# Optimization experiments

Hardware: AMD Instinct MI355X
Metric: run time of the kernel (lower is better)

## Reference

```python
import jax, jax.numpy as jnp
import numpy as np

G, NPG = 100, 500
N = G * NPG            # 50000 nodes, contiguous equal-size graphs
IN, H = 128, 256
L = 3                  # num_layers
K = 3                  # knn k (loop=True -> self included)
E = 16 * N             # 800000 edges

def setup_inputs():
    key = jax.random.key(0)
    k = jax.random.split(key, 8)
    x = jax.random.normal(k[0], (N, IN), jnp.float32)
    batch = jnp.repeat(jnp.arange(G, dtype=jnp.int32), NPG)
    gid = jax.random.randint(k[1], (E,), 0, G)
    src = jax.random.randint(k[2], (E,), 0, NPG) + gid * NPG
    dst = jax.random.randint(k[3], (E,), 0, NPG) + gid * NPG
    edge_index = jnp.stack([src, dst]).astype(jnp.int32)
    def lin(kk, fin, fout):
        return (jax.random.normal(kk, (fin, fout), jnp.float32) / np.sqrt(fin)).astype(jnp.float32)
    inp = dict(x=x, edge_index=edge_index, batch=batch)
    inp["emb_W"] = lin(k[4], IN, H); inp["emb_b"] = jnp.zeros((H,), jnp.float32)
    inp["conv_W"] = jnp.stack([lin(jax.random.fold_in(k[5], i), H, H) for i in range(L)])
    inp["conv_b"] = jnp.zeros((L, H), jnp.float32)
    inp["fconv_W"] = jnp.stack([lin(jax.random.fold_in(k[6], i), H, H) for i in range(L)])
    inp["fconv_b"] = jnp.zeros((L, H), jnp.float32)
    inp["norm_w"] = jnp.ones((L, H), jnp.float32); inp["norm_b"] = jnp.zeros((L, H), jnp.float32); inp["norm_ms"] = jnp.ones((L, H), jnp.float32)
    inp["fnorm_w"] = jnp.ones((L, H), jnp.float32); inp["fnorm_b"] = jnp.zeros((L, H), jnp.float32); inp["fnorm_ms"] = jnp.ones((L, H), jnp.float32)
    inp["gate_W"] = lin(k[7], 2 * H, H); inp["gate_b"] = jnp.zeros((H,), jnp.float32)
    return inp

def _gcn_conv(h, src, dst, W, b):
    # GCNConv: add self loops, symmetric deg^-1/2 normalization
    m = h @ W                                     # [N,H]
    loop = jnp.arange(N, dtype=src.dtype)
    s2 = jnp.concatenate([src, loop]); d2 = jnp.concatenate([dst, loop])
    deg = jax.ops.segment_sum(jnp.ones_like(d2, jnp.float32), d2, num_segments=N)
    dinv = jnp.where(deg > 0, jax.lax.rsqrt(deg), 0.0)
    coef = (dinv[s2] * dinv[d2])[:, None]
    return jax.ops.segment_sum(m[s2] * coef, d2, num_segments=N) + b

def _graph_norm(x, batch, w, b, ms, cnt):
    # PyG GraphNorm: out = w * (x - ms*mean) / sqrt(var + eps) + b, per-graph stats
    mean = jax.ops.segment_sum(x, batch, num_segments=G) / cnt
    out = x - mean[batch] * ms
    var = jax.ops.segment_sum(out * out, batch, num_segments=G) / cnt
    return w * out * jax.lax.rsqrt(var + 1e-5)[batch] + b

def _knn_graph(x):
    # per-graph cosine knn, loop=True (self has sim 1 and is kept)
    xr = x.reshape(G, NPG, -1)
    xn = xr / (jnp.linalg.norm(xr, axis=-1, keepdims=True) + 1e-12)
    sim = jnp.einsum('gnh,gmh->gnm', xn, xn)      # [G,NPG,NPG]
    _, idx = jax.lax.top_k(sim, K)                # [G,NPG,K]
    offs = (jnp.arange(G) * NPG)[:, None, None]
    src = (idx + offs).reshape(-1)
    dst = jnp.broadcast_to(jnp.arange(N).reshape(G, NPG, 1), (G, NPG, K)).reshape(-1)
    return src.astype(jnp.int32), dst.astype(jnp.int32)

def reference(x, edge_index, batch, emb_W, emb_b, conv_W, conv_b, norm_w, norm_b, norm_ms, fconv_W, fconv_b, fnorm_w, fnorm_b, fnorm_ms, gate_W, gate_b):
    cnt = jax.ops.segment_sum(jnp.ones((N,), jnp.float32), batch, num_segments=G)[:, None]
    h = x @ emb_W + emb_b
    fsrc, fdst = _knn_graph(h)
    src, dst = edge_index[0], edge_index[1]
    all_x = []
    for i in range(L - 1):   # eval mode: dropout is identity
        prev = h
        h = _gcn_conv(h, src, dst, conv_W[i], conv_b[i])
        h = jax.nn.leaky_relu(_graph_norm(h, batch, norm_w[i], norm_b[i], norm_ms[i], cnt))
        f = _gcn_conv(h, fsrc, fdst, fconv_W[i], fconv_b[i])
        f = jax.nn.leaky_relu(_graph_norm(f, batch, fnorm_w[i], fnorm_b[i], fnorm_ms[i], cnt))
        gate = jax.nn.sigmoid(jnp.concatenate([h, f], axis=-1) @ gate_W + gate_b)
        h = gate * h + (1.0 - gate) * f + prev
        all_x.append(h)
    # faithful to source: for i in range(L): += pool(all_x[i-1])  (Python negative indexing!)
    gf = jnp.zeros((G, H), jnp.float32)
    for i in range(L):
        gf = gf + jax.ops.segment_sum(all_x[i - 1], batch, num_segments=G) / cnt
    return gf
```

## Files before the change

kernel.cpp:

```cpp
#include <hip/hip_runtime.h>
#include <math.h>

#define NN 50000
#define GG 100
#define NPGc 500
#define HH 256
#define IND 128

typedef __attribute__((ext_vector_type(8))) short short8v;
typedef __attribute__((ext_vector_type(4))) float f32x4;

__device__ __forceinline__ ushort f2bf(float f) {
    union { float f; unsigned u; } v; v.f = f;
    unsigned r = (v.u + 0x7fffu + ((v.u >> 16) & 1u)) >> 16;
    return (ushort)r;
}
__device__ __forceinline__ float bf2f(ushort h) {
    union { unsigned u; float f; } v; v.u = ((unsigned)h) << 16;
    return v.f;
}

__device__ __forceinline__ int swz(int row, int kidx) { return kidx ^ ((row & 7) << 3); }

__global__ void wcvt(const float* __restrict__ src, ushort* __restrict__ dst, int K, int N)
{
    int i = blockIdx.x * 256 + threadIdx.x;
    if (i < K * N) {
        int n = i / K, k = i % K;
        dst[i] = f2bf(src[(size_t)k * N + n]);
    }
}

__global__ __launch_bounds__(256)
void gemm_mfma(const float* __restrict__ A, const float* __restrict__ A2,
               const ushort* __restrict__ Wt, const float* __restrict__ bias,
               float* __restrict__ C, ushort* __restrict__ Cbf,
               int M, int K, int lda, int mode,
               const float* __restrict__ hn, const float* __restrict__ fn,
               const float* __restrict__ prev)
{
    __shared__ ushort As[128][64];
    __shared__ ushort Bs[128][64];
    const int tid = threadIdx.x;
    const int lane = tid & 63;
    const int w = tid >> 6;
    const int wr = (w >> 1) * 64, wc = (w & 1) * 64;
    const int row0 = blockIdx.x * 128, col0 = blockIdx.y * 128;
    const int lr = lane & 15, lk = (lane >> 4) * 8;
    f32x4 acc[4][4] = {};

    for (int k0 = 0; k0 < K; k0 += 64) {
        __syncthreads();
        #pragma unroll
        for (int it = 0; it < 4; ++it) {
            int c = it * 256 + tid;
            int row = c >> 3, col = (c & 7) * 8;
            int gr = row0 + row; if (gr > M - 1) gr = M - 1;
            const float* Ap = A; int kk = k0 + col;
            if (A2 != nullptr && kk >= 256) { Ap = A2; kk -= 256; }
            const float* s = &Ap[(size_t)gr * lda + kk];
            float4 v0 = *(const float4*)s;
            float4 v1 = *(const float4*)(s + 4);
            union { ushort u[8]; int4 q; } pk;
            pk.u[0] = f2bf(v0.x); pk.u[1] = f2bf(v0.y); pk.u[2] = f2bf(v0.z); pk.u[3] = f2bf(v0.w);
            pk.u[4] = f2bf(v1.x); pk.u[5] = f2bf(v1.y); pk.u[6] = f2bf(v1.z); pk.u[7] = f2bf(v1.w);
            *(int4*)&As[row][swz(row, col)] = pk.q;
        }
        #pragma unroll
        for (int it = 0; it < 4; ++it) {
            int c = it * 256 + tid;
            int n = c >> 3, k = (c & 7) * 8;
            *(int4*)&Bs[n][swz(n, k)] = *(const int4*)&Wt[(size_t)(col0 + n) * K + k0 + k];
        }
        __syncthreads();
        #pragma unroll
        for (int ks = 0; ks < 2; ++ks) {
            short8v av[4], bv[4];
            #pragma unroll
            for (int m = 0; m < 4; ++m) {
                int rr = wr + m * 16 + lr;
                av[m] = *(const short8v*)&As[rr][swz(rr, ks * 32 + lk)];
            }
            #pragma unroll
            for (int n = 0; n < 4; ++n) {
                int rr = wc + n * 16 + lr;
                bv[n] = *(const short8v*)&Bs[rr][swz(rr, ks * 32 + lk)];
            }
            #pragma unroll
            for (int m = 0; m < 4; ++m)
                #pragma unroll
                for (int n = 0; n < 4; ++n)
                    acc[m][n] = __builtin_amdgcn_mfma_f32_16x16x32_bf16(av[m], bv[n], acc[m][n], 0, 0, 0);
        }
    }
    const int fr = (lane >> 4) * 4;
    if (mode == 0) {
        #pragma unroll
        for (int n = 0; n < 4; ++n) {
            int col = col0 + wc + n * 16 + lr;
            float bb = bias ? bias[col] : 0.f;
            #pragma unroll
            for (int m = 0; m < 4; ++m) {
                int rbase = row0 + wr + m * 16 + fr;
                #pragma unroll
                for (int r = 0; r < 4; ++r) {
                    int row = rbase + r;
                    if (row < M) C[(size_t)row * HH + col] = acc[m][n][r] + bb;
                }
            }
        }
    } else if (mode == 2) {
        #pragma unroll
        for (int n = 0; n < 4; ++n) {
            int col = col0 + wc + n * 16 + lr;
            float bb = bias ? bias[col] : 0.f;
            #pragma unroll
            for (int m = 0; m < 4; ++m) {
                int rbase = row0 + wr + m * 16 + fr;
                #pragma unroll
                for (int r = 0; r < 4; ++r) {
                    int row = rbase + r;
                    if (row < M) Cbf[(size_t)row * HH + col] = f2bf(acc[m][n][r] + bb);
                }
            }
        }
    } else {
        #pragma unroll
        for (int n = 0; n < 4; ++n) {
            int col = col0 + wc + n * 16 + lr;
            float gb = bias[col];
            #pragma unroll
            for (int m = 0; m < 4; ++m) {
                int rbase = row0 + wr + m * 16 + fr;
                #pragma unroll
                for (int r = 0; r < 4; ++r) {
                    int row = rbase + r;
                    if (row < M) {
                        size_t o = (size_t)row * HH + col;
                        float z = acc[m][n][r] + gb;
                        float s = 1.f / (1.f + expf(-z));
                        C[o] = s * hn[o] + (1.f - s) * fn[o] + prev[o];
                    }
                }
            }
        }
    }
}

__global__ __launch_bounds__(256)
void row_norm_hl(const float* __restrict__ h, ushort* __restrict__ xh, ushort* __restrict__ xl)
{
    int n = blockIdx.x, c = threadIdx.x;
    float v = h[(size_t)n * HH + c];
    __shared__ float red[256];
    red[c] = v * v;
    __syncthreads();
    for (int s = 128; s > 0; s >>= 1) {
        if (c < s) red[c] += red[c + s];
        __syncthreads();
    }
    float norm = sqrtf(red[0]);
    float xn = v / (norm + 1e-12f);
    ushort hi = f2bf(xn);
    xh[(size_t)n * HH + c] = hi;
    xl[(size_t)n * HH + c] = f2bf(xn - bf2f(hi));
}

__device__ __forceinline__ bool tk_better(float va, int ia, float vb, int ib)
{
    return (va > vb) || (va == vb && ia < ib);
}

__device__ __forceinline__ void ins3(float v, int i,
                                     float& a0, int& b0, float& a1, int& b1,
                                     float& a2, int& b2)
{
    if (tk_better(v, i, a0, b0))      { a2 = a1; b2 = b1; a1 = a0; b1 = b0; a0 = v; b0 = i; }
    else if (tk_better(v, i, a1, b1)) { a2 = a1; b2 = b1; a1 = v;  b1 = i; }
    else if (tk_better(v, i, a2, b2)) { a2 = v;  b2 = i; }
}

__device__ __forceinline__ void merge3(float& v0, float& v1, float& v2,
                                       int& i0, int& i1, int& i2, int off)
{
    float w0 = __shfl_xor(v0, off), w1 = __shfl_xor(v1, off), w2 = __shfl_xor(v2, off);
    int   j0 = __shfl_xor(i0, off), j1 = __shfl_xor(i1, off), j2 = __shfl_xor(i2, off);
    float avv[3] = { v0, v1, v2 }, bvv[3] = { w0, w1, w2 };
    int   aii[3] = { i0, i1, i2 }, bii[3] = { j0, j1, j2 };
    float rv[3]; int ri[3];
    int p = 0, q = 0;
    #pragma unroll
    for (int t = 0; t < 3; ++t) {
        bool takeA = tk_better(avv[p], aii[p], bvv[q], bii[q]);
        rv[t] = takeA ? avv[p] : bvv[q];
        ri[t] = takeA ? aii[p] : bii[q];
        if (takeA) ++p; else ++q;
    }
    v0 = rv[0]; v1 = rv[1]; v2 = rv[2];
    i0 = ri[0]; i1 = ri[1]; i2 = ri[2];
}

__global__ __launch_bounds__(256, 1)
void simtopk(const ushort* __restrict__ xnh, const ushort* __restrict__ xnl,
             int* __restrict__ fsrc)
{
    __shared__ ushort Bs[2][2][128][36];
    const int bid = blockIdx.x;
    const int xcd = bid & 7;
    const int rb  = (bid >> 3) & 7;
    const int g   = (bid >> 6) * 8 + xcd;
    if (g >= GG) return;
    const int row0 = rb * 64;
    const int tid  = threadIdx.x;
    const int lane = tid & 63;
    const int w    = tid >> 6;
    const int lr   = lane & 15;
    const int hi4  = lane >> 4;
    const size_t base = (size_t)g * NPGc * HH;

    int arow = row0 + w * 16 + lr; if (arow > NPGc - 1) arow = NPGc - 1;
    const ushort* aph = xnh + base + (size_t)arow * HH + hi4 * 8;
    const ushort* apl = xnl + base + (size_t)arow * HH + hi4 * 8;
    short8v ah[8], al[8];
    #pragma unroll
    for (int kc = 0; kc < 8; ++kc) {
        ah[kc] = *(const short8v*)(aph + kc * 32);
        al[kc] = *(const short8v*)(apl + kc * 32);
    }

    const int scol = tid >> 1;
    const int sq   = (tid & 1) * 2;

    float tv0[4], tv1[4], tv2[4];
    int   ti0[4], ti1[4], ti2[4];
    #pragma unroll
    for (int r = 0; r < 4; ++r) {
        tv0[r] = tv1[r] = tv2[r] = -2.f;
        ti0[r] = ti1[r] = ti2[r] = 0x7fffffff;
    }

    for (int ct = 0; ct < 4; ++ct) {
        const int col0 = ct * 128;
        int gcol = col0 + scol; if (gcol > NPGc - 1) gcol = NPGc - 1;
        const ushort* sph = xnh + base + (size_t)gcol * HH + sq * 8;
        const ushort* spl = xnl + base + (size_t)gcol * HH + sq * 8;

        {
            int4 h0 = *(const int4*)(sph);
            int4 h1 = *(const int4*)(sph + 8);
            int4 l0 = *(const int4*)(spl);
            int4 l1 = *(const int4*)(spl + 8);
            *(int4*)&Bs[0][0][scol][sq * 8]     = h0;
            *(int4*)&Bs[0][0][scol][sq * 8 + 8] = h1;
            *(int4*)&Bs[0][1][scol][sq * 8]     = l0;
            *(int4*)&Bs[0][1][scol][sq * 8 + 8] = l1;
        }
        __syncthreads();

        f32x4 acc[8] = {};
        #pragma unroll
        for (int kc = 0; kc < 8; ++kc) {
            const int cur = kc & 1, nxt = cur ^ 1;
            int4 h0, h1, l0, l1;
            if (kc < 7) {
                const ushort* nh = sph + (kc + 1) * 32;
                const ushort* nl = spl + (kc + 1) * 32;
                h0 = *(const int4*)(nh);
                h1 = *(const int4*)(nh + 8);
                l0 = *(const int4*)(nl);
                l1 = *(const int4*)(nl + 8);
            }
            short8v bh[8], bl[8];
            #pragma unroll
            for (int n = 0; n < 8; ++n) {
                int rr = n * 16 + lr;
                bh[n] = *(const short8v*)&Bs[cur][0][rr][hi4 * 8];
                bl[n] = *(const short8v*)&Bs[cur][1][rr][hi4 * 8];
            }
            #pragma unroll
            for (int n = 0; n < 8; ++n) {
                acc[n] = __builtin_amdgcn_mfma_f32_16x16x32_bf16(ah[kc], bh[n], acc[n], 0, 0, 0);
                acc[n] = __builtin_amdgcn_mfma_f32_16x16x32_bf16(ah[kc], bl[n], acc[n], 0, 0, 0);
                acc[n] = __builtin_amdgcn_mfma_f32_16x16x32_bf16(al[kc], bh[n], acc[n], 0, 0, 0);
            }
            if (kc < 7) {
                *(int4*)&Bs[nxt][0][scol][sq * 8]     = h0;
                *(int4*)&Bs[nxt][0][scol][sq * 8 + 8] = h1;
                *(int4*)&Bs[nxt][1][scol][sq * 8]     = l0;
                *(int4*)&Bs[nxt][1][scol][sq * 8 + 8] = l1;
            }
            __syncthreads();
        }

        #pragma unroll
        for (int n = 0; n < 8; ++n) {
            int col = col0 + n * 16 + lr;
            if (col < NPGc) {
                #pragma unroll
                for (int r = 0; r < 4; ++r)
                    ins3(acc[n][r], col, tv0[r], ti0[r], tv1[r], ti1[r], tv2[r], ti2[r]);
            }
        }
    }

    #pragma unroll
    for (int r = 0; r < 4; ++r) {
        #pragma unroll
        for (int off = 1; off <= 8; off <<= 1)
            merge3(tv0[r], tv1[r], tv2[r], ti0[r], ti1[r], ti2[r], off);
    }

    if (lr == 0) {
        #pragma unroll
        for (int r = 0; r < 4; ++r) {
            int row = row0 + w * 16 + hi4 * 4 + r;
            if (row < NPGc) {
                int rg = g * NPGc + row;
                fsrc[rg * 3 + 0] = g * NPGc + ti0[r];
                fsrc[rg * 3 + 1] = g * NPGc + ti1[r];
                fsrc[rg * 3 + 2] = g * NPGc + ti2[r];
            }
        }
    }
}

__global__ void hist_kernel(const int* __restrict__ dst, int* __restrict__ cnt, int nE)
{
    int e = blockIdx.x * 256 + threadIdx.x;
    if (e < nE) atomicAdd(&cnt[dst[e]], 1);
}

__global__ void scan1_kernel(const int* __restrict__ in, int* __restrict__ out,
                             int* __restrict__ bsum, int n)
{
    __shared__ int sh[256];
    int t = threadIdx.x;
    int i = blockIdx.x * 256 + t;
    int v = (i < n) ? in[i] : 0;
    sh[t] = v;
    __syncthreads();
    for (int s = 1; s < 256; s <<= 1) {
        int tv = (t >= s) ? sh[t - s] : 0;
        __syncthreads();
        sh[t] += tv;
        __syncthreads();
    }
    if (i < n) out[i] = sh[t] - v;
    if (t == 255) bsum[blockIdx.x] = sh[255];
}

__global__ void scan2_kernel(int* __restrict__ bsum, int nb)
{
    __shared__ int sh[256];
    int t = threadIdx.x;
    int v = (t < nb) ? bsum[t] : 0;
    sh[t] = v;
    __syncthreads();
    for (int s = 1; s < 256; s <<= 1) {
        int tv = (t >= s) ? sh[t - s] : 0;
        __syncthreads();
        sh[t] += tv;
        __syncthreads();
    }
    if (t < nb) bsum[t] = sh[t] - v;
}

__global__ void scan3_kernel(int* __restrict__ out, const int* __restrict__ bsum, int n)
{
    int i = blockIdx.x * 256 + threadIdx.x;
    if (i < n) out[i] += bsum[blockIdx.x];
}

__global__ void fill_kernel(const int* __restrict__ src, const int* __restrict__ dst,
                            const int* __restrict__ row_ptr, int* __restrict__ cursor,
                            int* __restrict__ sorted_src, int nE)
{
    int e = blockIdx.x * 256 + threadIdx.x;
    if (e < nE) {
        int d = dst[e];
        int pos = row_ptr[d] + atomicAdd(&cursor[d], 1);
        sorted_src[pos] = src[e];
    }
}

__global__ void dinv_kernel(const int* __restrict__ cnt, float* __restrict__ dinv, int n)
{
    int i = blockIdx.x * 256 + threadIdx.x;
    if (i < n) dinv[i] = rsqrtf((float)cnt[i] + 1.0f);
}

__global__ __launch_bounds__(256)
void gcn_gather(const ushort* __restrict__ m, const int* __restrict__ row_ptr,
                const int* __restrict__ cnt, const int* __restrict__ srcs,
                const float* __restrict__ dinv, const float* __restrict__ bias,
                float* __restrict__ out)
{
    int bid = blockIdx.x;
    int xcd = bid & 7, idx = bid >> 3;
    int g = xcd + 8 * (idx / NPGc);
    if (g >= GG) return;
    int n = g * NPGc + (idx % NPGc);
    int c = threadIdx.x;
    float dn = dinv[n];
    float acc = bf2f(m[(size_t)n * HH + c]) * dn;
    int s0 = row_ptr[n], e0 = s0 + cnt[n];
    for (int e = s0; e < e0; ++e) {
        int s = srcs[e];
        acc += bf2f(m[(size_t)s * HH + c]) * dinv[s];
    }
    out[(size_t)n * HH + c] = acc * dn + bias[c];
}

__global__ __launch_bounds__(256)
void fgcn_gather(const ushort* __restrict__ m, const int* __restrict__ fsrc,
                 const float* __restrict__ bias, float* __restrict__ out)
{
    int bid = blockIdx.x;
    int xcd = bid & 7, idx = bid >> 3;
    int g = xcd + 8 * (idx / NPGc);
    if (g >= GG) return;
    int n = g * NPGc + (idx % NPGc);
    int c = threadIdx.x;
    int s0 = fsrc[n * 3], s1 = fsrc[n * 3 + 1], s2 = fsrc[n * 3 + 2];
    float acc = bf2f(m[(size_t)n * HH + c]) + bf2f(m[(size_t)s0 * HH + c])
              + bf2f(m[(size_t)s1 * HH + c]) + bf2f(m[(size_t)s2 * HH + c]);
    out[(size_t)n * HH + c] = 0.25f * acc + bias[c];
}

__global__ __launch_bounds__(256)
void norm_stats(const float* __restrict__ x, float* __restrict__ S1, float* __restrict__ S2)
{
    int g = blockIdx.x, chunk = blockIdx.y, c = threadIdx.x;
    int r0 = chunk * 63, r1 = min(r0 + 63, NPGc);
    float s1 = 0.f, s2 = 0.f;
    for (int r = r0; r < r1; ++r) {
        float v = x[((size_t)(g * NPGc + r)) * HH + c];
        s1 += v; s2 += v * v;
    }
    atomicAdd(&S1[g * HH + c], s1);
    atomicAdd(&S2[g * HH + c], s2);
}

__global__ __launch_bounds__(256)
void norm_apply(float* __restrict__ x, const float* __restrict__ S1, const float* __restrict__ S2,
                const float* __restrict__ w, const float* __restrict__ b,
                const float* __restrict__ ms)
{
    int n = blockIdx.x, c = threadIdx.x;
    int g = n / NPGc;
    size_t o = (size_t)n * HH + c;
    float v = x[o];
    float mean = S1[g * HH + c] / (float)NPGc;
    float mm = mean * ms[c];
    float var = S2[g * HH + c] / (float)NPGc - 2.f * mm * mean + mm * mm;
    float outv = w[c] * (v - mm) * rsqrtf(var + 1e-5f) + b[c];
    x[o] = outv > 0.f ? outv : 0.01f * outv;
}

__global__ __launch_bounds__(256)
void pool_kernel(const float* __restrict__ X0, const float* __restrict__ X1,
                 float* __restrict__ out)
{
    int g = blockIdx.x, c = threadIdx.x;
    float s0 = 0.f, s1 = 0.f;
    for (int r = 0; r < NPGc; ++r) {
        size_t o = ((size_t)(g * NPGc + r)) * HH + c;
        s0 += X0[o];
        s1 += X1[o];
    }
    out[g * HH + c] = (s0 + 2.f * s1) / (float)NPGc;
}

__global__ void sentinel_kernel(float* out, int n)
{
    int i = blockIdx.x * 256 + threadIdx.x;
    if (i < n) out[i] = 12345.0f;
}

extern "C" void kernel_launch(void* const* d_in, const int* in_sizes, int n_in,
                              void* d_out, int out_size, void* d_ws, size_t ws_size,
                              hipStream_t stream)
{
    const float* x       = (const float*)d_in[0];
    const int* edge_idx  = (const int*)d_in[1];
    const float* emb_W   = (const float*)d_in[3];
    const float* emb_b   = (const float*)d_in[4];
    const float* conv_W  = (const float*)d_in[5];
    const float* conv_b  = (const float*)d_in[6];
    const float* fconv_W = (const float*)d_in[7];
    const float* fconv_b = (const float*)d_in[8];
    const float* norm_w  = (const float*)d_in[9];
    const float* norm_b  = (const float*)d_in[10];
    const float* norm_ms = (const float*)d_in[11];
    const float* fnorm_w = (const float*)d_in[12];
    const float* fnorm_b = (const float*)d_in[13];
    const float* fnorm_ms= (const float*)d_in[14];
    const float* gate_W  = (const float*)d_in[15];
    const float* gate_b  = (const float*)d_in[16];

    const int E = in_sizes[1] / 2;
    const int* esrc = edge_idx;
    const int* edst = edge_idx + E;

    const size_t NHf = (size_t)NN * HH;
    char* p = (char*)d_ws;
    auto alloc = [&](size_t bytes) { char* r = p; p += (bytes + 255) & ~(size_t)255; return r; };
    float* B0 = (float*)alloc(NHf * 4);
    float* B1 = (float*)alloc(NHf * 4);
    float* B2 = (float*)alloc(NHf * 4);
    float* B3 = (float*)alloc(NHf * 4);
    ushort* xnh = (ushort*)B2;
    ushort* xnl = xnh + NHf;
    ushort* msgbf = (ushort*)alloc(NHf * 2);
    int* sorted_src = (int*)alloc((size_t)E * 4);
    int* row_ptr    = (int*)alloc((size_t)NN * 4);
    int* deg_cnt    = (int*)alloc((size_t)NN * 4);
    int* cursor     = (int*)alloc((size_t)NN * 4);
    float* dinv     = (float*)alloc((size_t)NN * 4);
    int* fsrc       = (int*)alloc((size_t)NN * 3 * 4);
    float* S1       = (float*)alloc((size_t)GG * HH * 4);
    float* S2       = (float*)alloc((size_t)GG * HH * 4);
    int* bsum       = (int*)alloc(1024);
    ushort* wts     = (ushort*)alloc((size_t)425984 * 2);
    size_t needed = (size_t)(p - (char*)d_ws);
    if (ws_size < needed) {
        sentinel_kernel<<<(out_size + 255) / 256, 256, 0, stream>>>((float*)d_out, out_size);
        return;
    }
    ushort* embWt   = wts;
    ushort* convWt0 = wts + 32768;
    ushort* convWt1 = wts + 32768 + 65536;
    ushort* fconvWt0 = wts + 163840;
    ushort* fconvWt1 = wts + 163840 + 65536;
    ushort* gateWt  = wts + 294912;

    const int nScanB = (NN + 255) / 256;
    const int gatherGrid = 8 * 13 * NPGc;

    hipMemsetAsync(deg_cnt, 0, (size_t)NN * 4, stream);
    hipMemsetAsync(cursor, 0, (size_t)NN * 4, stream);

    wcvt<<<(32768 + 255) / 256, 256, 0, stream>>>(emb_W, embWt, IND, HH);
    wcvt<<<(65536 + 255) / 256, 256, 0, stream>>>(conv_W, convWt0, HH, HH);
    wcvt<<<(65536 + 255) / 256, 256, 0, stream>>>(conv_W + 65536, convWt1, HH, HH);
    wcvt<<<(65536 + 255) / 256, 256, 0, stream>>>(fconv_W, fconvWt0, HH, HH);
    wcvt<<<(65536 + 255) / 256, 256, 0, stream>>>(fconv_W + 65536, fconvWt1, HH, HH);
    wcvt<<<(131072 + 255) / 256, 256, 0, stream>>>(gate_W, gateWt, 2 * HH, HH);

    dim3 ggrid((NN + 127) / 128, 2);
    gemm_mfma<<<ggrid, 256, 0, stream>>>(x, nullptr, embWt, emb_b, B0, nullptr,
                                         NN, IND, IND, 0, nullptr, nullptr, nullptr);

    hist_kernel<<<(E + 255) / 256, 256, 0, stream>>>(edst, deg_cnt, E);
    scan1_kernel<<<nScanB, 256, 0, stream>>>(deg_cnt, row_ptr, bsum, NN);
    scan2_kernel<<<1, 256, 0, stream>>>(bsum, nScanB);
    scan3_kernel<<<nScanB, 256, 0, stream>>>(row_ptr, bsum, NN);
    fill_kernel<<<(E + 255) / 256, 256, 0, stream>>>(esrc, edst, row_ptr, cursor, sorted_src, E);
    dinv_kernel<<<(NN + 255) / 256, 256, 0, stream>>>(deg_cnt, dinv, NN);

    row_norm_hl<<<NN, 256, 0, stream>>>(B0, xnh, xnl);
    simtopk<<<832, 256, 0, stream>>>(xnh, xnl, fsrc);

    float* h  = B0;
    float* mb = B1;
    dim3 ngrid(GG, 8);
    for (int i = 0; i < 2; ++i) {
        const ushort* Wc = (i == 0) ? convWt0 : convWt1;
        const ushort* Wf = (i == 0) ? fconvWt0 : fconvWt1;
        const float* bc  = conv_b  + (size_t)i * HH;
        const float* bf  = fconv_b + (size_t)i * HH;
        gemm_mfma<<<ggrid, 256, 0, stream>>>(h, nullptr, Wc, nullptr, nullptr, msgbf,
                                             NN, HH, HH, 2, nullptr, nullptr, nullptr);
        gcn_gather<<<gatherGrid, 256, 0, stream>>>(msgbf, row_ptr, deg_cnt, sorted_src,
                                                   dinv, bc, B2);
        hipMemsetAsync(S1, 0, (size_t)2 * GG * HH * 4, stream);
        norm_stats<<<ngrid, 256, 0, stream>>>(B2, S1, S2);
        norm_apply<<<NN, 256, 0, stream>>>(B2, S1, S2, norm_w + i * HH, norm_b + i * HH,
                                           norm_ms + i * HH);
        gemm_mfma<<<ggrid, 256, 0, stream>>>(B2, nullptr, Wf, nullptr, nullptr, msgbf,
                                             NN, HH, HH, 2, nullptr, nullptr, nullptr);
        fgcn_gather<<<gatherGrid, 256, 0, stream>>>(msgbf, fsrc, bf, B3);
        hipMemsetAsync(S1, 0, (size_t)2 * GG * HH * 4, stream);
        norm_stats<<<ngrid, 256, 0, stream>>>(B3, S1, S2);
        norm_apply<<<NN, 256, 0, stream>>>(B3, S1, S2, fnorm_w + i * HH, fnorm_b + i * HH,
                                           fnorm_ms + i * HH);
        gemm_mfma<<<ggrid, 256, 0, stream>>>(B2, B3, gateWt, gate_b, mb, nullptr,
                                             NN, 2 * HH, HH, 1, B2, B3, h);
        float* t = h; h = mb; mb = t;
    }
    pool_kernel<<<GG, 256, 0, stream>>>(mb, h, (float*)d_out);
}
```

Measured before the change: 1.296 ms.

## Restructure kNN similarity GEMM into LDS-staged swizzled K-tiles with two blocks per CU

The simtopk kernel no longer keeps the whole A row fragment (hi and lo bf16 splits over K=256) in registers with a double-buffered B ring. Both A and B tiles are now staged through XOR-swizzled shared memory in K chunks of 64, and launch bounds allow two blocks per CU. This is meant to cut register pressure and LDS bank conflicts so occupancy can rise. In exchange the A tile is reloaded from global memory once per column tile, and prefetch overlap is lost because each K chunk is loaded and then consumed between two barriers.

```diff
diff --git a/kernel.cpp b/kernel.cpp
--- a/kernel.cpp
+++ b/kernel.cpp
@@ -200,11 +200,12 @@
     i0 = ri[0]; i1 = ri[1]; i2 = ri[2];
 }
 
-__global__ __launch_bounds__(256, 1)
+__global__ __launch_bounds__(256, 2)
 void simtopk(const ushort* __restrict__ xnh, const ushort* __restrict__ xnl,
              int* __restrict__ fsrc)
 {
-    __shared__ ushort Bs[2][2][128][36];
+    __shared__ ushort Ash[64][64], Asl[64][64];
+    __shared__ ushort Bsh[128][64], Bsl[128][64];
     const int bid = blockIdx.x;
     const int xcd = bid & 7;
     const int rb  = (bid >> 3) & 7;
@@ -216,20 +217,8 @@
     const int w    = tid >> 6;
     const int lr   = lane & 15;
     const int hi4  = lane >> 4;
+    const int lk   = hi4 * 8;
     const size_t base = (size_t)g * NPGc * HH;
-
-    int arow = row0 + w * 16 + lr; if (arow > NPGc - 1) arow = NPGc - 1;
-    const ushort* aph = xnh + base + (size_t)arow * HH + hi4 * 8;
-    const ushort* apl = xnl + base + (size_t)arow * HH + hi4 * 8;
-    short8v ah[8], al[8];
-    #pragma unroll
-    for (int kc = 0; kc < 8; ++kc) {
-        ah[kc] = *(const short8v*)(aph + kc * 32);
-        al[kc] = *(const short8v*)(apl + kc * 32);
-    }
-
-    const int scol = tid >> 1;
-    const int sq   = (tid & 1) * 2;
 
     float tv0[4], tv1[4], tv2[4];
     int   ti0[4], ti1[4], ti2[4];
@@ -241,84 +230,73 @@
 
     for (int ct = 0; ct < 4; ++ct) {
         const int col0 = ct * 128;
-        int gcol = col0 + scol; if (gcol > NPGc - 1) gcol = NPGc - 1;
-        const ushort* sph = xnh + base + (size_t)gcol * HH + sq * 8;
-        const ushort* spl = xnl + base + (size_t)gcol * HH + sq * 8;
-
-        {
-            int4 h0 = *(const int4*)(sph);
-            int4 h1 = *(const int4*)(sph + 8);
-            int4 l0 = *(const int4*)(spl);
-            int4 l1 = *(const int4*)(spl + 8);
-            *(int4*)&Bs[0][0][scol][sq * 8]     = h0;
-            *(int4*)&Bs[0][0][scol][sq * 8 + 8] = h1;
-            *(int4*)&Bs[0][1][scol][sq * 8]     = l0;
-            *(int4*)&Bs[0][1][scol][sq * 8 + 8] = l1;
-        }
-        __syncthreads();
-
         f32x4 acc[8] = {};
-        #pragma unroll
-        for (int kc = 0; kc < 8; ++kc) {
-            const int cur = kc & 1, nxt = cur ^ 1;
-            int4 h0, h1, l0, l1;
-            if (kc < 7) {
-                const ushort* nh = sph + (kc + 1) * 32;
-                const ushort* nl = spl + (kc + 1) * 32;
-                h0 = *(const int4*)(nh);
-                h1 = *(const int4*)(nh + 8);
-                l0 = *(const int4*)(nl);
-                l1 = *(const int4*)(nl + 8);
-            }
-            short8v bh[8], bl[8];
+        for (int k0 = 0; k0 < HH; k0 += 64) {
+            __syncthreads();
+            #pragma unroll
+            for (int it = 0; it < 2; ++it) {
+                int flat = it * 256 + tid;
+                int row = flat >> 3, col = (flat & 7) * 8;
+                int grow = row0 + row; if (grow > NPGc - 1) grow = NPGc - 1;
+                size_t o = base + (size_t)grow * HH + k0 + col;
+                *(int4*)&Ash[row][swz(row, col)] = *(const int4*)(xnh + o);
+                *(int4*)&Asl[row][swz(row, col)] = *(const int4*)(xnl + o);
+            }
+            #pragma unroll
+            for (int it = 0; it < 4; ++it) {
+                int flat = it * 256 + tid;
+                int row = flat >> 3, col = (flat & 7) * 8;
+                int gcol = col0 + row; if (gcol > NPGc - 1) gcol = NPGc - 1;
+                size_t o = base + (size_t)gcol * HH + k0 + col;
+                *(int4*)&Bsh[row][swz(row, col)] = *(const int4*)(xnh + o);
+                *(int4*)&Bsl[row][swz(row, col)] = *(const int4*)(xnl + o);
+            }
+            __syncthreads();
+            #pragma unroll
+            for (int ks = 0; ks < 2; ++ks) {
+                const int ra = w * 16 + lr;
+                short8v ah = *(const short8v*)&Ash[ra][swz(ra, ks * 32 + lk)];
+                short8v al = *(const short8v*)&Asl[ra][swz(ra, ks * 32 + lk)];
+                #pragma unroll
+                for (int n = 0; n < 8; ++n) {
+                    const int rbn = n * 16 + lr;
+                    short8v bh = *(const short8v*)&Bsh[rbn][swz(rbn, ks * 32 + lk)];
+                    short8v bl = *(const short8v*)&Bsl[rbn][swz(rbn, ks * 32 + lk)];
+                    acc[n] = __builtin_amdgcn_mfma_f32_16x16x32_bf16(ah, bh, acc[n], 0, 0, 0);
+                    acc[n] = __builtin_amdgcn_mfma_f32_16x16x32_bf16(ah, bl, acc[n], 0, 0, 0);
+                    acc[n] = __builtin_amdgcn_mfma_f32_16x16x32_bf16(al, bh, acc[n], 0, 0, 0);
+                }
+            }
+        }
+        #pragma unroll
+        for (int r = 0; r < 4; ++r) {
+            float a0 = tv0[r], a1 = tv1[r], a2 = tv2[r];
+            int   b0 = ti0[r], b1 = ti1[r], b2 = ti2[r];
             #pragma unroll
             for (int n = 0; n < 8; ++n) {
-                int rr = n * 16 + lr;
-                bh[n] = *(const short8v*)&Bs[cur][0][rr][hi4 * 8];
-                bl[n] = *(const short8v*)&Bs[cur][1][rr][hi4 * 8];
-            }
-            #pragma unroll
-            for (int n = 0; n < 8; ++n) {
-                acc[n] = __builtin_amdgcn_mfma_f32_16x16x32_bf16(ah[kc], bh[n], acc[n], 0, 0, 0);
-                acc[n] = __builtin_amdgcn_mfma_f32_16x16x32_bf16(ah[kc], bl[n], acc[n], 0, 0, 0);
-                acc[n] = __builtin_amdgcn_mfma_f32_16x16x32_bf16(al[kc], bh[n], acc[n], 0, 0, 0);
-            }
-            if (kc < 7) {
-                *(int4*)&Bs[nxt][0][scol][sq * 8]     = h0;
-                *(int4*)&Bs[nxt][0][scol][sq * 8 + 8] = h1;
-                *(int4*)&Bs[nxt][1][scol][sq * 8]     = l0;
-                *(int4*)&Bs[nxt][1][scol][sq * 8 + 8] = l1;
-            }
-            __syncthreads();
-        }
-
-        #pragma unroll
-        for (int n = 0; n < 8; ++n) {
-            int col = col0 + n * 16 + lr;
-            if (col < NPGc) {
-                #pragma unroll
-                for (int r = 0; r < 4; ++r)
-                    ins3(acc[n][r], col, tv0[r], ti0[r], tv1[r], ti1[r], tv2[r], ti2[r]);
-            }
+                int col = col0 + n * 16 + lr;
+                if (col < NPGc)
+                    ins3(acc[n][r], col, a0, b0, a1, b1, a2, b2);
+            }
+            tv0[r] = a0; tv1[r] = a1; tv2[r] = a2;
+            ti0[r] = b0; ti1[r] = b1; ti2[r] = b2;
         }
     }
 
     #pragma unroll
     for (int r = 0; r < 4; ++r) {
+        float a0 = tv0[r], a1 = tv1[r], a2 = tv2[r];
+        int   b0 = ti0[r], b1 = ti1[r], b2 = ti2[r];
         #pragma unroll
         for (int off = 1; off <= 8; off <<= 1)
-            merge3(tv0[r], tv1[r], tv2[r], ti0[r], ti1[r], ti2[r], off);
-    }
-
-    if (lr == 0) {
-        #pragma unroll
-        for (int r = 0; r < 4; ++r) {
+            merge3(a0, a1, a2, b0, b1, b2, off);
+        if (lr == 0) {
             int row = row0 + w * 16 + hi4 * 4 + r;
             if (row < NPGc) {
                 int rg = g * NPGc + row;
-                fsrc[rg * 3 + 0] = g * NPGc + ti0[r];
-                fsrc[rg * 3 + 1] = g * NPGc + ti1[r];
-                fsrc[rg * 3 + 2] = g * NPGc + ti2[r];
+                fsrc[rg * 3 + 0] = g * NPGc + b0;
+                fsrc[rg * 3 + 1] = g * NPGc + b1;
+                fsrc[rg * 3 + 2] = g * NPGc + b2;
             }
         }
     }
```

Result: slower. 1.322 ms (+2.0%).

## Store intermediate activations in bf16 and replace norm atomics with partial sums

Applied to the files above, without the earlier changes.

Intermediate activations (GCN gather outputs, normalized features, gated layer outputs) are now stored as bf16 instead of fp32. The GEMM reads bf16 inputs directly with no conversion, which roughly halves memory traffic across the gather, norm, gate and pool kernels. GraphNorm statistics are written as per-chunk partial sums that norm_apply reduces, removing the atomics and memsets. The topk insertion loop is also reordered per row. The cost is extra rounding to bf16 on stored activations, including the residual path.

```diff
diff --git a/kernel.cpp b/kernel.cpp
--- a/kernel.cpp
+++ b/kernel.cpp
@@ -32,12 +32,12 @@
 }
 
 __global__ __launch_bounds__(256)
-void gemm_mfma(const float* __restrict__ A, const float* __restrict__ A2,
+void gemm_mfma(const void* __restrict__ Av, const void* __restrict__ A2v, int abf,
                const ushort* __restrict__ Wt, const float* __restrict__ bias,
                float* __restrict__ C, ushort* __restrict__ Cbf,
                int M, int K, int lda, int mode,
-               const float* __restrict__ hn, const float* __restrict__ fn,
-               const float* __restrict__ prev)
+               const ushort* __restrict__ hn, const ushort* __restrict__ fn,
+               const void* __restrict__ prevv, int prevbf)
 {
     __shared__ ushort As[128][64];
     __shared__ ushort Bs[128][64];
@@ -56,15 +56,23 @@
             int c = it * 256 + tid;
             int row = c >> 3, col = (c & 7) * 8;
             int gr = row0 + row; if (gr > M - 1) gr = M - 1;
-            const float* Ap = A; int kk = k0 + col;
-            if (A2 != nullptr && kk >= 256) { Ap = A2; kk -= 256; }
-            const float* s = &Ap[(size_t)gr * lda + kk];
-            float4 v0 = *(const float4*)s;
-            float4 v1 = *(const float4*)(s + 4);
-            union { ushort u[8]; int4 q; } pk;
-            pk.u[0] = f2bf(v0.x); pk.u[1] = f2bf(v0.y); pk.u[2] = f2bf(v0.z); pk.u[3] = f2bf(v0.w);
-            pk.u[4] = f2bf(v1.x); pk.u[5] = f2bf(v1.y); pk.u[6] = f2bf(v1.z); pk.u[7] = f2bf(v1.w);
-            *(int4*)&As[row][swz(row, col)] = pk.q;
+            int kk = k0 + col;
+            if (abf) {
+                const ushort* Ap = (const ushort*)Av;
+                if (A2v != nullptr && kk >= 256) { Ap = (const ushort*)A2v; kk -= 256; }
+                *(int4*)&As[row][swz(row, col)] =
+                    *(const int4*)&Ap[(size_t)gr * lda + kk];
+            } else {
+                const float* Ap = (const float*)Av;
+                if (A2v != nullptr && kk >= 256) { Ap = (const float*)A2v; kk -= 256; }
+                const float* s = &Ap[(size_t)gr * lda + kk];
+                float4 v0 = *(const float4*)s;
+                float4 v1 = *(const float4*)(s + 4);
+                union { ushort u[8]; int4 q; } pk;
+                pk.u[0] = f2bf(v0.x); pk.u[1] = f2bf(v0.y); pk.u[2] = f2bf(v0.z); pk.u[3] = f2bf(v0.w);
+                pk.u[4] = f2bf(v1.x); pk.u[5] = f2bf(v1.y); pk.u[6] = f2bf(v1.z); pk.u[7] = f2bf(v1.w);
+                *(int4*)&As[row][swz(row, col)] = pk.q;
+            }
         }
         #pragma unroll
         for (int it = 0; it < 4; ++it) {
@@ -139,7 +147,11 @@
                         size_t o = (size_t)row * HH + col;
                         float z = acc[m][n][r] + gb;
                         float s = 1.f / (1.f + expf(-z));
-                        C[o] = s * hn[o] + (1.f - s) * fn[o] + prev[o];
+                        float hv = bf2f(hn[o]);
+                        float fv = bf2f(fn[o]);
+                        float pv = prevbf ? bf2f(((const ushort*)prevv)[o])
+                                          : ((const float*)prevv)[o];
+                        Cbf[o] = f2bf(s * hv + (1.f - s) * fv + pv);
                     }
                 }
             }
@@ -293,32 +305,34 @@
         }
 
         #pragma unroll
-        for (int n = 0; n < 8; ++n) {
-            int col = col0 + n * 16 + lr;
-            if (col < NPGc) {
-                #pragma unroll
-                for (int r = 0; r < 4; ++r)
-                    ins3(acc[n][r], col, tv0[r], ti0[r], tv1[r], ti1[r], tv2[r], ti2[r]);
-            }
+        for (int r = 0; r < 4; ++r) {
+            float a0 = tv0[r], a1 = tv1[r], a2 = tv2[r];
+            int   b0 = ti0[r], b1 = ti1[r], b2 = ti2[r];
+            #pragma unroll
+            for (int n = 0; n < 8; ++n) {
+                int col = col0 + n * 16 + lr;
+                if (col < NPGc)
+                    ins3(acc[n][r], col, a0, b0, a1, b1, a2, b2);
+            }
+            tv0[r] = a0; tv1[r] = a1; tv2[r] = a2;
+            ti0[r] = b0; ti1[r] = b1; ti2[r] = b2;
         }
     }
 
     #pragma unroll
     for (int r = 0; r < 4; ++r) {
+        float a0 = tv0[r], a1 = tv1[r], a2 = tv2[r];
+        int   b0 = ti0[r], b1 = ti1[r], b2 = ti2[r];
         #pragma unroll
         for (int off = 1; off <= 8; off <<= 1)
-            merge3(tv0[r], tv1[r], tv2[r], ti0[r], ti1[r], ti2[r], off);
-    }
-
-    if (lr == 0) {
-        #pragma unroll
-        for (int r = 0; r < 4; ++r) {
+            merge3(a0, a1, a2, b0, b1, b2, off);
+        if (lr == 0) {
             int row = row0 + w * 16 + hi4 * 4 + r;
             if (row < NPGc) {
                 int rg = g * NPGc + row;
-                fsrc[rg * 3 + 0] = g * NPGc + ti0[r];
-                fsrc[rg * 3 + 1] = g * NPGc + ti1[r];
-                fsrc[rg * 3 + 2] = g * NPGc + ti2[r];
+                fsrc[rg * 3 + 0] = g * NPGc + b0;
+                fsrc[rg * 3 + 1] = g * NPGc + b1;
+                fsrc[rg * 3 + 2] = g * NPGc + b2;
             }
         }
     }
@@ -393,7 +407,7 @@
 void gcn_gather(const ushort* __restrict__ m, const int* __restrict__ row_ptr,
                 const int* __restrict__ cnt, const int* __restrict__ srcs,
                 const float* __restrict__ dinv, const float* __restrict__ bias,
-                float* __restrict__ out)
+                ushort* __restrict__ out)
 {
     int bid = blockIdx.x;
     int xcd = bid & 7, idx = bid >> 3;
@@ -408,12 +422,12 @@
         int s = srcs[e];
         acc += bf2f(m[(size_t)s * HH + c]) * dinv[s];
     }
-    out[(size_t)n * HH + c] = acc * dn + bias[c];
+    out[(size_t)n * HH + c] = f2bf(acc * dn + bias[c]);
 }
 
 __global__ __launch_bounds__(256)
 void fgcn_gather(const ushort* __restrict__ m, const int* __restrict__ fsrc,
-                 const float* __restrict__ bias, float* __restrict__ out)
+                 const float* __restrict__ bias, ushort* __restrict__ out)
 {
     int bid = blockIdx.x;
     int xcd = bid & 7, idx = bid >> 3;
@@ -424,49 +438,57 @@
     int s0 = fsrc[n * 3], s1 = fsrc[n * 3 + 1], s2 = fsrc[n * 3 + 2];
     float acc = bf2f(m[(size_t)n * HH + c]) + bf2f(m[(size_t)s0 * HH + c])
               + bf2f(m[(size_t)s1 * HH + c]) + bf2f(m[(size_t)s2 * HH + c]);
-    out[(size_t)n * HH + c] = 0.25f * acc + bias[c];
+    out[(size_t)n * HH + c] = f2bf(0.25f * acc + bias[c]);
 }
 
 __global__ __launch_bounds__(256)
-void norm_stats(const float* __restrict__ x, float* __restrict__ S1, float* __restrict__ S2)
+void norm_stats(const ushort* __restrict__ x, float* __restrict__ S1p, float* __restrict__ S2p)
 {
     int g = blockIdx.x, chunk = blockIdx.y, c = threadIdx.x;
     int r0 = chunk * 63, r1 = min(r0 + 63, NPGc);
     float s1 = 0.f, s2 = 0.f;
     for (int r = r0; r < r1; ++r) {
-        float v = x[((size_t)(g * NPGc + r)) * HH + c];
+        float v = bf2f(x[((size_t)(g * NPGc + r)) * HH + c]);
         s1 += v; s2 += v * v;
     }
-    atomicAdd(&S1[g * HH + c], s1);
-    atomicAdd(&S2[g * HH + c], s2);
+    size_t o = ((size_t)(g * 8 + chunk)) * HH + c;
+    S1p[o] = s1;
+    S2p[o] = s2;
 }
 
 __global__ __launch_bounds__(256)
-void norm_apply(float* __restrict__ x, const float* __restrict__ S1, const float* __restrict__ S2,
+void norm_apply(ushort* __restrict__ x, const float* __restrict__ S1p, const float* __restrict__ S2p,
                 const float* __restrict__ w, const float* __restrict__ b,
                 const float* __restrict__ ms)
 {
     int n = blockIdx.x, c = threadIdx.x;
     int g = n / NPGc;
     size_t o = (size_t)n * HH + c;
-    float v = x[o];
-    float mean = S1[g * HH + c] / (float)NPGc;
+    float v = bf2f(x[o]);
+    float s1 = 0.f, s2 = 0.f;
+    #pragma unroll
+    for (int j = 0; j < 8; ++j) {
+        size_t po = ((size_t)(g * 8 + j)) * HH + c;
+        s1 += S1p[po];
+        s2 += S2p[po];
+    }
+    float mean = s1 / (float)NPGc;
     float mm = mean * ms[c];
-    float var = S2[g * HH + c] / (float)NPGc - 2.f * mm * mean + mm * mm;
+    float var = s2 / (float)NPGc - 2.f * mm * mean + mm * mm;
     float outv = w[c] * (v - mm) * rsqrtf(var + 1e-5f) + b[c];
-    x[o] = outv > 0.f ? outv : 0.01f * outv;
+    x[o] = f2bf(outv > 0.f ? outv : 0.01f * outv);
 }
 
 __global__ __launch_bounds__(256)
-void pool_kernel(const float* __restrict__ X0, const float* __restrict__ X1,
+void pool_kernel(const ushort* __restrict__ X0, const ushort* __restrict__ X1,
                  float* __restrict__ out)
 {
     int g = blockIdx.x, c = threadIdx.x;
     float s0 = 0.f, s1 = 0.f;
     for (int r = 0; r < NPGc; ++r) {
         size_t o = ((size_t)(g * NPGc + r)) * HH + c;
-        s0 += X0[o];
-        s1 += X1[o];
+        s0 += bf2f(X0[o]);
+        s1 += bf2f(X1[o]);
     }
     out[g * HH + c] = (s0 + 2.f * s1) / (float)NPGc;
 }
@@ -505,21 +527,22 @@
     const size_t NHf = (size_t)NN * HH;
     char* p = (char*)d_ws;
     auto alloc = [&](size_t bytes) { char* r = p; p += (bytes + 255) & ~(size_t)255; return r; };
-    float* B0 = (float*)alloc(NHf * 4);
-    float* B1 = (float*)alloc(NHf * 4);
-    float* B2 = (float*)alloc(NHf * 4);
-    float* B3 = (float*)alloc(NHf * 4);
-    ushort* xnh = (ushort*)B2;
-    ushort* xnl = xnh + NHf;
-    ushort* msgbf = (ushort*)alloc(NHf * 2);
+    float*  B0 = (float*)alloc(NHf * 4);
+    ushort* Mr = (ushort*)alloc(NHf * 2);
+    ushort* Ar = (ushort*)alloc(NHf * 2);
+    ushort* Br = (ushort*)alloc(NHf * 2);
+    ushort* H0 = (ushort*)alloc(NHf * 2);
+    ushort* H1 = (ushort*)alloc(NHf * 2);
+    ushort* xnh = Mr;
+    ushort* xnl = Ar;
     int* sorted_src = (int*)alloc((size_t)E * 4);
     int* row_ptr    = (int*)alloc((size_t)NN * 4);
     int* deg_cnt    = (int*)alloc((size_t)NN * 4);
     int* cursor     = (int*)alloc((size_t)NN * 4);
     float* dinv     = (float*)alloc((size_t)NN * 4);
     int* fsrc       = (int*)alloc((size_t)NN * 3 * 4);
-    float* S1       = (float*)alloc((size_t)GG * HH * 4);
-    float* S2       = (float*)alloc((size_t)GG * HH * 4);
+    float* S1p      = (float*)alloc((size_t)GG * 8 * HH * 4);
+    float* S2p      = (float*)alloc((size_t)GG * 8 * HH * 4);
     int* bsum       = (int*)alloc(1024);
     ushort* wts     = (ushort*)alloc((size_t)425984 * 2);
     size_t needed = (size_t)(p - (char*)d_ws);
@@ -548,8 +571,8 @@
     wcvt<<<(131072 + 255) / 256, 256, 0, stream>>>(gate_W, gateWt, 2 * HH, HH);
 
     dim3 ggrid((NN + 127) / 128, 2);
-    gemm_mfma<<<ggrid, 256, 0, stream>>>(x, nullptr, embWt, emb_b, B0, nullptr,
-                                         NN, IND, IND, 0, nullptr, nullptr, nullptr);
+    gemm_mfma<<<ggrid, 256, 0, stream>>>(x, nullptr, 0, embWt, emb_b, B0, nullptr,
+                                         NN, IND, IND, 0, nullptr, nullptr, nullptr, 0);
 
     hist_kernel<<<(E + 255) / 256, 256, 0, stream>>>(edst, deg_cnt, E);
     scan1_kernel<<<nScanB, 256, 0, stream>>>(deg_cnt, row_ptr, bsum, NN);
@@ -561,32 +584,32 @@
     row_norm_hl<<<NN, 256, 0, stream>>>(B0, xnh, xnl);
     simtopk<<<832, 256, 0, stream>>>(xnh, xnl, fsrc);
 
-    float* h  = B0;
-    float* mb = B1;
     dim3 ngrid(GG, 8);
+    const void* hptr = (const void*)B0;
+    int habf = 0;
+    ushort* Hout[2] = { H0, H1 };
     for (int i = 0; i < 2; ++i) {
         const ushort* Wc = (i == 0) ? convWt0 : convWt1;
         const ushort* Wf = (i == 0) ? fconvWt0 : fconvWt1;
         const float* bc  = conv_b  + (size_t)i * HH;
         const float* bf  = fconv_b + (size_t)i * HH;
-        gemm_mfma<<<ggrid, 256, 0, stream>>>(h, nullptr, Wc, nullptr, nullptr, msgbf,
-                                             NN, HH, HH, 2, nullptr, nullptr, nullptr);
-        gcn_gather<<<gatherGrid, 256, 0, stream>>>(msgbf, row_ptr, deg_cnt, sorted_src,
-                                                   dinv, bc, B2);
-        hipMemsetAsync(S1, 0, (size_t)2 * GG * HH * 4, stream);
-        norm_stats<<<ngrid, 256, 0, stream>>>(B2, S1, S2);
-        norm_apply<<<NN, 256, 0, stream>>>(B2, S1, S2, norm_w + i * HH, norm_b + i * HH,
+        gemm_mfma<<<ggrid, 256, 0, stream>>>(hptr, nullptr, habf, Wc, nullptr, nullptr, Mr,
+                                             NN, HH, HH, 2, nullptr, nullptr, nullptr, 0);
+        gcn_gather<<<gatherGrid, 256, 0, stream>>>(Mr, row_ptr, deg_cnt, sorted_src,
+                                                   dinv, bc, Ar);
+        norm_stats<<<ngrid, 256, 0, stream>>>(Ar, S1p, S2p);
+        norm_apply<<<NN, 256, 0, stream>>>(Ar, S1p, S2p, norm_w + i * HH, norm_b + i * HH,
                                            norm_ms + i * HH);
-        gemm_mfma<<<ggrid, 256, 0, stream>>>(B2, nullptr, Wf, nullptr, nullptr, msgbf,
-                                             NN, HH, HH, 2, nullptr, nullptr, nullptr);
-        fgcn_gather<<<gatherGrid, 256, 0, stream>>>(msgbf, fsrc, bf, B3);
-        hipMemsetAsync(S1, 0, (size_t)2 * GG * HH * 4, stream);
-        norm_stats<<<ngrid, 256, 0, stream>>>(B3, S1, S2);
-        norm_apply<<<NN, 256, 0, stream>>>(B3, S1, S2, fnorm_w + i * HH, fnorm_b + i * HH,
+        gemm_mfma<<<ggrid, 256, 0, stream>>>(Ar, nullptr, 1, Wf, nullptr, nullptr, Mr,
+                                             NN, HH, HH, 2, nullptr, nullptr, nullptr, 0);
+        fgcn_gather<<<gatherGrid, 256, 0, stream>>>(Mr, fsrc, bf, Br);
+        norm_stats<<<ngrid, 256, 0, stream>>>(Br, S1p, S2p);
+        norm_apply<<<NN, 256, 0, stream>>>(Br, S1p, S2p, fnorm_w + i * HH, fnorm_b + i * HH,
                                            fnorm_ms + i * HH);
-        gemm_mfma<<<ggrid, 256, 0, stream>>>(B2, B3, gateWt, gate_b, mb, nullptr,
-                                             NN, 2 * HH, HH, 1, B2, B3, h);
-        float* t = h; h = mb; mb = t;
-    }
-    pool_kernel<<<GG, 256, 0, stream>>>(mb, h, (float*)d_out);
-}
+        gemm_mfma<<<ggrid, 256, 0, stream>>>(Ar, Br, 1, gateWt, gate_b, nullptr, Hout[i],
+                                             NN, 2 * HH, HH, 1, Ar, Br, hptr, habf);
+        hptr = (const void*)Hout[i];
+        habf = 1;
+    }
+    pool_kernel<<<GG, 256, 0, stream>>>(H0, H1, (float*)d_out);
+}
```

After: 1.321 ms. No clear change (+1.9%).
